# Kernel tuning notes

Measured on AMD Instinct MI355X. Metric: run time of the kernel, lower is better.

## Reference

```python
import jax, jax.numpy as jnp
import numpy as np

B = 16384
EPS = 1e-5
DIMS = [(3072, 4096), (4096, 4096), (4096, 256), (256, 16), (16, 16), (16, 10)]


def binarize(v):
    # BNN binarization with straight-through semantics (matches .data assignment in torch)
    return v + jax.lax.stop_gradient(jnp.sign(v) - v)


def blinear(x, w, b):
    # BinarizeLinear: binarize input (in_dim != 784) and weights, float bias add
    return binarize(x) @ binarize(w).T + b


def batchnorm(x, g, b):
    m = x.mean(axis=0)
    v = x.var(axis=0)
    return (x - m) * jax.lax.rsqrt(v + EPS) * g + b


def hardtanh(x):
    return jnp.clip(x, -1.0, 1.0)


def setup_inputs() -> dict:
    key = jax.random.key(0)
    ks = jax.random.split(key, 20)
    inp = {"x": jax.random.normal(ks[0], (B, 3072), dtype=jnp.float32)}
    for i, (din, dout) in enumerate(DIMS):
        inp[f"w{i}"] = jax.random.normal(ks[1 + 2 * i], (dout, din), dtype=jnp.float32) * 0.05
        inp[f"b{i}"] = jax.random.normal(ks[2 + 2 * i], (dout,), dtype=jnp.float32) * 0.01
    # BatchNorm affine params for layers after blinear 0,1,2 and final (dims 4096,4096,256,10)
    for j, d in enumerate([4096, 4096, 256, 10]):
        inp[f"g{j}"] = jnp.ones((d,), dtype=jnp.float32)
        inp[f"be{j}"] = jnp.zeros((d,), dtype=jnp.float32)
    return inp


def reference(x, w0, b0, w1, b1, w2, b2, w3, b3, w4, b4, w5, b5,
              g0, be0, g1, be1, g2, be2, g3, be3):
    h = x.reshape(-1, 3072)
    h = hardtanh(batchnorm(blinear(h, w0, b0), g0, be0))
    h = hardtanh(batchnorm(blinear(h, w1, b1), g1, be1))
    h = hardtanh(batchnorm(blinear(h, w2, b2), g2, be2))
    h = hardtanh(blinear(h, w3, b3))
    h = hardtanh(blinear(h, w4, b4))
    h = batchnorm(blinear(h, w5, b5), g3, be3)
    return jax.nn.log_softmax(h, axis=-1)
```

## Files before the change

### kernel.cpp

```cpp
#include <hip/hip_runtime.h>
#include <stdint.h>

typedef int v4i __attribute__((ext_vector_type(4)));
typedef int v8i __attribute__((ext_vector_type(8)));
typedef float v4f __attribute__((ext_vector_type(4)));
typedef short v8s __attribute__((ext_vector_type(8)));
typedef unsigned long long ull;
typedef unsigned int uint;

#define GLOAD16(g, l)                                                          \
  __builtin_amdgcn_global_load_lds(                                            \
      (const __attribute__((address_space(1))) void*)(g),                      \
      (__attribute__((address_space(3))) void*)(l), 16, 0, 0)

__device__ __forceinline__ signed char sgnf(float v) {
  return v > 0.f ? (signed char)1 : (v < 0.f ? (signed char)-1 : (signed char)0);
}
__device__ __forceinline__ uint nib(float v) {
  return v > 0.f ? 2u : (v < 0.f ? 10u : 0u);
}

__global__ void k_bin(const float4* __restrict__ in, char4* __restrict__ out, int n4) {
  int i = blockIdx.x * blockDim.x + threadIdx.x;
  int stride = gridDim.x * blockDim.x;
  for (; i < n4; i += stride) {
    float4 v = in[i];
    char4 o;
    o.x = sgnf(v.x); o.y = sgnf(v.y); o.z = sgnf(v.z); o.w = sgnf(v.w);
    out[i] = o;
  }
}

__global__ void k_binp(const float4* __restrict__ in, uint* __restrict__ out, int n8) {
  int i = blockIdx.x * blockDim.x + threadIdx.x;
  int stride = gridDim.x * blockDim.x;
  for (; i < n8; i += stride) {
    float4 a = in[i * 2], b = in[i * 2 + 1];
    out[i] = nib(a.x) | (nib(a.y) << 4) | (nib(a.z) << 8) | (nib(a.w) << 12) |
             (nib(b.x) << 16) | (nib(b.y) << 20) | (nib(b.z) << 24) | (nib(b.w) << 28);
  }
}

#define BM 128
#define BN 128

template <int K, int N>
__global__ __launch_bounds__(256, 2) void k_bgemm(
    const unsigned char* __restrict__ X, const unsigned char* __restrict__ W,
    short* __restrict__ A, ull* __restrict__ S, int M)
{
  __shared__ __align__(16) unsigned char As[BM * 128];
  __shared__ __align__(16) unsigned char Bs[BN * 128];
  constexpr int Kb = K >> 1;
  constexpr int NT = K / 256;
  constexpr int NBX = N / BN;
  const int t = threadIdx.x;
  const int lane = t & 63;
  const int wave = t >> 6;
  const int wm = wave >> 1, wn = wave & 1;

  const int wg = blockIdx.x;
  const int bm = (wg / NBX) * BM, bn = (wg % NBX) * BN;

  const int srow = lane >> 3;
  const int sslot = (lane & 7);

  const unsigned char* Xb0 = X + (size_t)bm * Kb;
  const unsigned char* Wb0 = W + (size_t)bn * Kb;

  v4f acc[4][4] = {};
  v8i a8[4], b8[4];
#pragma unroll
  for (int m = 0; m < 4; ++m) { a8[m] = (v8i)(0); b8[m] = (v8i)(0); }

  const unsigned char* gx[4];
  const unsigned char* gw[4];
  int ldsoff[4];
#pragma unroll
  for (int c = 0; c < 4; ++c) {
    int br = (wave * 4 + c) * 8;
    int row = br + srow;
    int ss = sslot ^ (row & 7);
    gx[c] = Xb0 + (size_t)row * Kb + ss * 16;
    gw[c] = Wb0 + (size_t)row * Kb + ss * 16;
    ldsoff[c] = br * 128;
  }
  int aoff[4], boff[4];
#pragma unroll
  for (int m = 0; m < 4; ++m) {
    int arow = wm * 64 + m * 16 + (lane & 15);
    aoff[m] = arow * 128 + (((lane >> 4) ^ (arow & 7)) * 16);
    int brow = wn * 64 + m * 16 + (lane & 15);
    boff[m] = brow * 128 + (((lane >> 4) ^ (brow & 7)) * 16);
  }

#pragma unroll
  for (int tile = 0; tile < NT; ++tile) {
#pragma unroll
    for (int c = 0; c < 4; ++c) {
      GLOAD16(gx[c] + tile * 128, As + ldsoff[c]);
      GLOAD16(gw[c] + tile * 128, Bs + ldsoff[c]);
    }
    __syncthreads();
#pragma unroll
    for (int kk = 0; kk < 2; ++kk) {
#pragma unroll
      for (int m = 0; m < 4; ++m) {
        v4i tmp = *(const v4i*)(As + (aoff[m] ^ (kk << 6)));
        a8[m][0] = tmp[0]; a8[m][1] = tmp[1]; a8[m][2] = tmp[2]; a8[m][3] = tmp[3];
      }
#pragma unroll
      for (int n = 0; n < 4; ++n) {
        v4i tmp = *(const v4i*)(Bs + (boff[n] ^ (kk << 6)));
        b8[n][0] = tmp[0]; b8[n][1] = tmp[1]; b8[n][2] = tmp[2]; b8[n][3] = tmp[3];
      }
#pragma unroll
      for (int m = 0; m < 4; ++m)
#pragma unroll
        for (int n = 0; n < 4; ++n)
          acc[m][n] = __builtin_amdgcn_mfma_scale_f32_16x16x128_f8f6f4(
              a8[m], b8[n], acc[m][n], 4 , 4 ,
              0, 0x7F7F7F7Fu, 0, 0x7F7F7F7Fu);
    }
    __syncthreads();
  }

#pragma unroll
  for (int m = 0; m < 4; ++m) {
    int rbase = bm + wm * 64 + m * 16 + (lane >> 4) * 4;
#pragma unroll
    for (int n = 0; n < 4; ++n) {
      int col = bn + wn * 64 + n * 16 + (lane & 15);
#pragma unroll
      for (int r = 0; r < 4; ++r)
        __builtin_nontemporal_store((short)(int)acc[m][n][r],
                                    A + (size_t)(rbase + r) * N + col);
    }
  }

#pragma unroll
  for (int n = 0; n < 4; ++n) {
    int s = 0, q = 0;
#pragma unroll
    for (int m = 0; m < 4; ++m)
#pragma unroll
      for (int r = 0; r < 4; ++r) {
        int v = (int)acc[m][n][r];
        s += v; q += v * v;
      }
    s += __shfl_xor(s, 16); s += __shfl_xor(s, 32);
    q += __shfl_xor(q, 16); q += __shfl_xor(q, 32);
    if ((lane >> 4) == 0) {
      int col = bn + wn * 64 + n * 16 + (lane & 15);
      atomicAdd(&S[col], (ull)(long long)s);
      atomicAdd(&S[(size_t)N + col], (ull)(long long)q);
    }
  }
}

__global__ void k_finalize(const ull* __restrict__ sums, const float* __restrict__ g,
                           int M, int N, float* __restrict__ meanf, float* __restrict__ sgf) {
  int j = blockIdx.x * blockDim.x + threadIdx.x;
  if (j >= N) return;
  double sum = (double)(long long)sums[j];
  double sumsq = (double)(long long)sums[N + j];
  double mean = sum / (double)M;
  double var = sumsq / (double)M - mean * mean;
  if (var < 0.0) var = 0.0;
  double inv = 1.0 / sqrt(var + 1e-5);
  meanf[j] = (float)mean;
  sgf[j] = (float)(inv * (double)g[j]);
}

__global__ void k_signbn_pack(const short* __restrict__ A, const float* __restrict__ meanf,
                              const float* __restrict__ sgf, const float* __restrict__ be,
                              uint* __restrict__ Xp, int total8, int nmask) {
  int i = blockIdx.x * blockDim.x + threadIdx.x;
  int stride = gridDim.x * blockDim.x;
  for (; i < total8; i += stride) {
    v8s a = __builtin_nontemporal_load((const v8s*)(A + (size_t)i * 8));
    int c0 = (i * 8) & nmask;
    uint b = 0;
#pragma unroll
    for (int j = 0; j < 8; ++j) {
      float z = ((float)a[j] - meanf[c0 + j]) * sgf[c0 + j] + be[c0 + j];
      b |= nib(z) << (4 * j);
    }
    Xp[i] = b;
  }
}

__global__ void k_signbn(const short4* __restrict__ A4, const float* __restrict__ meanf,
                         const float* __restrict__ sgf, const float* __restrict__ be,
                         char4* __restrict__ X4, int total4, int nmask) {
  int i = blockIdx.x * blockDim.x + threadIdx.x;
  int stride = gridDim.x * blockDim.x;
  for (; i < total4; i += stride) {
    short4 a = A4[i];
    int c0 = (i * 4) & nmask;
    char4 o;
    o.x = sgnf(((float)a.x - meanf[c0    ]) * sgf[c0    ] + be[c0    ]);
    o.y = sgnf(((float)a.y - meanf[c0 + 1]) * sgf[c0 + 1] + be[c0 + 1]);
    o.z = sgnf(((float)a.z - meanf[c0 + 2]) * sgf[c0 + 2] + be[c0 + 2]);
    o.w = sgnf(((float)a.w - meanf[c0 + 3]) * sgf[c0 + 3] + be[c0 + 3]);
    X4[i] = o;
  }
}

__global__ __launch_bounds__(256) void k_tail(
    const signed char* __restrict__ X3, const signed char* __restrict__ W3,
    const signed char* __restrict__ W4, const signed char* __restrict__ W5,
    const float* __restrict__ b3, const float* __restrict__ b4,
    int* __restrict__ A5, ull* __restrict__ sums5, int M)
{
  __shared__ __align__(16) signed char sW3[16 * 256];
  __shared__ __align__(16) signed char sW4[256];
  __shared__ __align__(16) signed char sW5[160];
  __shared__ __align__(16) signed char sX[16 * 256];
  __shared__ signed char sH[16][16];
  __shared__ int bsum[10], bsq[10];
  int t = threadIdx.x;
  int rowBlock = blockIdx.x * 16;
  ((int4*)sW3)[t] = ((const int4*)W3)[t];
  ((int4*)sX)[t] = ((const int4*)(X3 + (size_t)rowBlock * 256))[t];
  if (t < 16) ((int4*)sW4)[t] = ((const int4*)W4)[t];
  if (t < 10) {
    ((int4*)sW5)[t] = ((const int4*)W5)[t];
    bsum[t] = 0; bsq[t] = 0;
  }
  __syncthreads();
  int r = t >> 4, j = t & 15;
  int d3 = 0;
#pragma unroll 8
  for (int k = 0; k < 256; ++k) d3 += (int)sX[r * 256 + k] * (int)sW3[j * 256 + k];
  sH[r][j] = sgnf((float)d3 + b3[j]);
  __syncthreads();
  int d4 = 0;
#pragma unroll
  for (int k = 0; k < 16; ++k) d4 += (int)sH[r][k] * (int)sW4[j * 16 + k];
  signed char x5 = sgnf((float)d4 + b4[j]);
  __syncthreads();
  sH[r][j] = x5;
  __syncthreads();
  if (j < 10) {
    int d5 = 0;
#pragma unroll
    for (int k = 0; k < 16; ++k) d5 += (int)sH[r][k] * (int)sW5[j * 16 + k];
    A5[(size_t)(rowBlock + r) * 10 + j] = d5;
    atomicAdd(&bsum[j], d5);
    atomicAdd(&bsq[j], d5 * d5);
  }
  __syncthreads();
  if (t < 10) {
    atomicAdd(&sums5[t], (ull)(long long)bsum[t]);
    atomicAdd(&sums5[10 + t], (ull)(long long)bsq[t]);
  }
}

__global__ void k_lsm(const int* __restrict__ A5, const float* __restrict__ meanf,
                      const float* __restrict__ sgf, const float* __restrict__ be,
                      float* __restrict__ out, int M) {
  int r = blockIdx.x * blockDim.x + threadIdx.x;
  if (r >= M) return;
  float tv[10]; float mx = -3.0e38f;
#pragma unroll
  for (int j = 0; j < 10; ++j) {
    tv[j] = ((float)A5[(size_t)r * 10 + j] - meanf[j]) * sgf[j] + be[j];
    mx = fmaxf(mx, tv[j]);
  }
  float s = 0.f;
#pragma unroll
  for (int j = 0; j < 10; ++j) s += expf(tv[j] - mx);
  float lse = mx + logf(s);
#pragma unroll
  for (int j = 0; j < 10; ++j) out[(size_t)r * 10 + j] = tv[j] - lse;
}

extern "C" void kernel_launch(void* const* d_in, const int* in_sizes, int n_in,
                              void* d_out, int out_size, void* d_ws, size_t ws_size,
                              hipStream_t stream) {
  const float* x   = (const float*)d_in[0];
  const float* w0f = (const float*)d_in[1];
  const float* w1f = (const float*)d_in[3];
  const float* w2f = (const float*)d_in[5];
  const float* w3f = (const float*)d_in[7];  const float* b3f = (const float*)d_in[8];
  const float* w4f = (const float*)d_in[9];  const float* b4f = (const float*)d_in[10];
  const float* w5f = (const float*)d_in[11];
  const float* g0 = (const float*)d_in[13]; const float* be0 = (const float*)d_in[14];
  const float* g1 = (const float*)d_in[15]; const float* be1 = (const float*)d_in[16];
  const float* g2 = (const float*)d_in[17]; const float* be2 = (const float*)d_in[18];
  const float* g3 = (const float*)d_in[19]; const float* be3 = (const float*)d_in[20];

  const int M = in_sizes[0] / 3072;
  char* w = (char*)d_ws;
  short* Abuf          = (short*)w;
  unsigned char* X0p   = (unsigned char*)(w + 134217728);
  unsigned char* Xbp   = (unsigned char*)(w + 184549376);
  signed char* X3      = (signed char*)(w + 251658240);
  unsigned char* Ws0p  = (unsigned char*)(w + 255852544);
  unsigned char* Ws1p  = (unsigned char*)(w + 268435456);
  unsigned char* Ws2p  = (unsigned char*)(w + 285212672);
  signed char* Ws3 = (signed char*)(w + 286261248);
  signed char* Ws4 = (signed char*)(w + 286265344);
  signed char* Ws5 = (signed char*)(w + 286265600);
  int* A5          = (int*)(w + 286265856);
  ull* S0          = (ull*)(w + 286921216);
  ull* S1          = (ull*)(w + 286986752);
  ull* S2          = (ull*)(w + 287052288);
  ull* S5          = (ull*)(w + 287056384);
  float* P0m = (float*)(w + 287056640); float* P0s = (float*)(w + 287073024);
  float* P1m = (float*)(w + 287089408); float* P1s = (float*)(w + 287105792);
  float* P2m = (float*)(w + 287122176); float* P2s = (float*)(w + 287123200);
  float* P5m = (float*)(w + 287124224); float* P5s = (float*)(w + 287124288);

  hipMemsetAsync(w + 286921216, 0, 135424, stream);

  auto binp = [&](const float* src, unsigned char* dst, int n) {
    int n8 = n / 8;
    int grid = (n8 + 255) / 256; if (grid > 8192) grid = 8192;
    k_binp<<<grid, 256, 0, stream>>>((const float4*)src, (uint*)dst, n8);
  };
  binp(x,   X0p,  M * 3072);
  binp(w0f, Ws0p, 4096 * 3072);
  binp(w1f, Ws1p, 4096 * 4096);
  binp(w2f, Ws2p, 256 * 4096);
  k_bin<<<1, 64, 0, stream>>>((const float4*)w3f, (char4*)Ws3, 16 * 256 / 4);
  k_bin<<<1, 64, 0, stream>>>((const float4*)w4f, (char4*)Ws4, 16 * 16 / 4);
  k_bin<<<1, 40, 0, stream>>>((const float4*)w5f, (char4*)Ws5, 10 * 16 / 4);

  k_bgemm<3072, 4096><<<(4096 / BN) * (M / BM), 256, 0, stream>>>(X0p, Ws0p, Abuf, S0, M);
  k_finalize<<<16, 256, 0, stream>>>(S0, g0, M, 4096, P0m, P0s);
  k_signbn_pack<<<8192, 256, 0, stream>>>(Abuf, P0m, P0s, be0, (uint*)Xbp, M * 4096 / 8, 4095);

  k_bgemm<4096, 4096><<<(4096 / BN) * (M / BM), 256, 0, stream>>>(Xbp, Ws1p, Abuf, S1, M);
  k_finalize<<<16, 256, 0, stream>>>(S1, g1, M, 4096, P1m, P1s);
  k_signbn_pack<<<8192, 256, 0, stream>>>(Abuf, P1m, P1s, be1, (uint*)Xbp, M * 4096 / 8, 4095);

  k_bgemm<4096, 256><<<(256 / BN) * (M / BM), 256, 0, stream>>>(Xbp, Ws2p, Abuf, S2, M);
  k_finalize<<<1, 256, 0, stream>>>(S2, g2, M, 256, P2m, P2s);
  k_signbn<<<4096, 256, 0, stream>>>((const short4*)Abuf, P2m, P2s, be2, (char4*)X3, M * 256 / 4, 255);

  k_tail<<<M / 16, 256, 0, stream>>>(X3, Ws3, Ws4, Ws5, b3f, b4f, A5, S5, M);
  k_finalize<<<1, 32, 0, stream>>>(S5, g3, M, 10, P5m, P5s);
  k_lsm<<<(M + 255) / 256, 256, 0, stream>>>(A5, P5m, P5s, be3, (float*)d_out, M);

  (void)n_in; (void)out_size; (void)ws_size;
}
```

Measured before the change: 481.7 us.

## Add 256x256 8-wave FP4 GEMM with double-buffered LDS pipeline for big layers

```diff
diff --git a/kernel.cpp b/kernel.cpp
--- a/kernel.cpp
+++ b/kernel.cpp
@@ -12,6 +12,12 @@
   __builtin_amdgcn_global_load_lds(                                            \
       (const __attribute__((address_space(1))) void*)(g),                      \
       (__attribute__((address_space(3))) void*)(l), 16, 0, 0)
+
+__device__ __forceinline__ void bar() {
+  asm volatile("" ::: "memory");
+  __builtin_amdgcn_s_barrier();
+  asm volatile("" ::: "memory");
+}
 
 __device__ __forceinline__ signed char sgnf(float v) {
   return v > 0.f ? (signed char)1 : (v < 0.f ? (signed char)-1 : (signed char)0);
@@ -38,6 +44,161 @@
     float4 a = in[i * 2], b = in[i * 2 + 1];
     out[i] = nib(a.x) | (nib(a.y) << 4) | (nib(a.z) << 8) | (nib(a.w) << 12) |
              (nib(b.x) << 16) | (nib(b.y) << 20) | (nib(b.z) << 24) | (nib(b.w) << 28);
+  }
+}
+
+#define BM2 256
+#define BN2 256
+
+template <int K, int N>
+__global__ __launch_bounds__(512, 2) void k_bgemm2(
+    const unsigned char* __restrict__ X, const unsigned char* __restrict__ W,
+    short* __restrict__ A, ull* __restrict__ S, int M)
+{
+  __shared__ __align__(16) unsigned char lds[2][2][BM2 * 128];
+  constexpr int Kb = K >> 1;
+  constexpr int NT = K / 256;
+  constexpr int NBX = N / BN2;
+  const int t512 = threadIdx.x;
+  const int lane = t512 & 63;
+  const int wave = t512 >> 6;
+  const int wm = wave >> 2;
+  const int wn = wave & 3;
+  const int wg = blockIdx.x;
+  const int bm = (wg / NBX) * BM2, bn = (wg % NBX) * BN2;
+
+  const int srow = lane >> 3;
+  const int ssl = (lane & 7) ^ (srow & 7);
+
+  const unsigned char* gA[2][2];
+  const unsigned char* gB[2][2];
+  int ldst[2][2];
+#pragma unroll
+  for (int h = 0; h < 2; ++h)
+#pragma unroll
+    for (int c = 0; c < 2; ++c) {
+      int row = h * 128 + c * 64 + wave * 8 + srow;
+      gA[h][c] = X + (size_t)(bm + row) * Kb + ssl * 16;
+      gB[h][c] = W + (size_t)(bn + row) * Kb + ssl * 16;
+      ldst[h][c] = (h * 128 + c * 64 + wave * 8) * 128;
+    }
+
+  auto stageA = [&](int h, int buf, int tt) {
+    GLOAD16(gA[h][0] + tt * 128, &lds[buf][0][ldst[h][0]]);
+    GLOAD16(gA[h][1] + tt * 128, &lds[buf][0][ldst[h][1]]);
+  };
+  auto stageB = [&](int h, int buf, int tt) {
+    GLOAD16(gB[h][0] + tt * 128, &lds[buf][1][ldst[h][0]]);
+    GLOAD16(gB[h][1] + tt * 128, &lds[buf][1][ldst[h][1]]);
+  };
+
+  int aoff[8], boff[4];
+#pragma unroll
+  for (int m = 0; m < 8; ++m) {
+    int r = wm * 128 + m * 16 + (lane & 15);
+    aoff[m] = r * 128 + (((lane >> 4) ^ (r & 7)) * 16);
+  }
+#pragma unroll
+  for (int n = 0; n < 4; ++n) {
+    int r = wn * 64 + n * 16 + (lane & 15);
+    boff[n] = r * 128 + (((lane >> 4) ^ (r & 7)) * 16);
+  }
+
+  v4f acc[8][4] = {};
+  v8i a8[4][2], b8[4][2];
+#pragma unroll
+  for (int i = 0; i < 4; ++i)
+#pragma unroll
+    for (int kk = 0; kk < 2; ++kk) { a8[i][kk] = (v8i)(0); b8[i][kk] = (v8i)(0); }
+
+#define RD_A(mh, Ap)                                                           \
+  _Pragma("unroll") for (int mq = 0; mq < 4; ++mq)                             \
+    _Pragma("unroll") for (int kk = 0; kk < 2; ++kk) {                         \
+      v4i tmp = *(const v4i*)((Ap) + (aoff[(mh) * 4 + mq] ^ (kk << 6)));       \
+      a8[mq][kk][0] = tmp[0]; a8[mq][kk][1] = tmp[1];                          \
+      a8[mq][kk][2] = tmp[2]; a8[mq][kk][3] = tmp[3]; }
+#define RD_B(nh, Bp)                                                           \
+  _Pragma("unroll") for (int nq = 0; nq < 2; ++nq)                             \
+    _Pragma("unroll") for (int kk = 0; kk < 2; ++kk) {                         \
+      v4i tmp = *(const v4i*)((Bp) + (boff[(nh) * 2 + nq] ^ (kk << 6)));       \
+      b8[(nh) * 2 + nq][kk][0] = tmp[0]; b8[(nh) * 2 + nq][kk][1] = tmp[1];    \
+      b8[(nh) * 2 + nq][kk][2] = tmp[2]; b8[(nh) * 2 + nq][kk][3] = tmp[3]; }
+#define QUAD(mh, nh)                                                           \
+  { __builtin_amdgcn_s_setprio(1);                                             \
+    _Pragma("unroll") for (int mq = 0; mq < 4; ++mq)                           \
+      _Pragma("unroll") for (int nq = 0; nq < 2; ++nq)                         \
+        _Pragma("unroll") for (int kk = 0; kk < 2; ++kk)                       \
+          acc[(mh) * 4 + mq][(nh) * 2 + nq] =                                  \
+              __builtin_amdgcn_mfma_scale_f32_16x16x128_f8f6f4(                \
+                  a8[mq][kk], b8[(nh) * 2 + nq][kk],                           \
+                  acc[(mh) * 4 + mq][(nh) * 2 + nq],                           \
+                  4, 4, 0, 0x7F7F7F7Fu, 0, 0x7F7F7F7Fu);                       \
+    __builtin_amdgcn_s_setprio(0); }
+
+  stageA(0, 0, 0); stageB(0, 0, 0); stageA(1, 0, 0); stageB(1, 0, 0);
+  stageB(0, 1, 1); stageA(0, 1, 1);
+  asm volatile("s_waitcnt vmcnt(4)" ::: "memory");
+  bar();
+
+#pragma unroll 2
+  for (int t = 0; t < NT; ++t) {
+    const int p = t & 1, q = p ^ 1;
+    const unsigned char* Ap = &lds[p][0][0];
+    const unsigned char* Bp = &lds[p][1][0];
+    RD_A(0, Ap); RD_B(0, Bp);
+    if (t + 1 < NT) stageA(1, q, t + 1);
+    bar(); QUAD(0, 0); bar();
+    RD_B(1, Bp);
+    if (t + 1 < NT) stageB(1, q, t + 1);
+    bar(); QUAD(0, 1); bar();
+    RD_A(1, Ap);
+    if (t + 2 < NT) stageB(0, p, t + 2);
+    bar(); QUAD(1, 0); bar();
+    if (t + 2 < NT) {
+      stageA(0, p, t + 2);
+      asm volatile("s_waitcnt vmcnt(4)" ::: "memory");
+    } else {
+      asm volatile("s_waitcnt vmcnt(0)" ::: "memory");
+    }
+    bar(); QUAD(1, 1); bar();
+  }
+#undef RD_A
+#undef RD_B
+#undef QUAD
+
+#pragma unroll
+  for (int m = 0; m < 8; ++m) {
+    int rbase = bm + wm * 128 + m * 16 + (lane >> 4) * 4;
+#pragma unroll
+    for (int n = 0; n < 4; ++n) {
+      int col = bn + wn * 64 + n * 16 + (lane & 15);
+#pragma unroll
+      for (int r = 0; r < 4; ++r)
+        __builtin_nontemporal_store((short)(int)acc[m][n][r],
+                                    A + (size_t)(rbase + r) * N + col);
+    }
+  }
+
+#pragma unroll
+  for (int n = 0; n < 4; ++n) {
+    int s = 0; long long q64 = 0;
+#pragma unroll
+    for (int m = 0; m < 8; ++m) {
+      int qq = 0;
+#pragma unroll
+      for (int r = 0; r < 4; ++r) {
+        int v = (int)acc[m][n][r];
+        s += v; qq += v * v;
+      }
+      q64 += qq;
+    }
+    s += __shfl_xor(s, 16); s += __shfl_xor(s, 32);
+    q64 += __shfl_xor(q64, 16); q64 += __shfl_xor(q64, 32);
+    if ((lane >> 4) == 0) {
+      int col = bn + wn * 64 + n * 16 + (lane & 15);
+      atomicAdd(&S[col], (ull)(long long)s);
+      atomicAdd(&S[(size_t)N + col], (ull)q64);
+    }
   }
 }
 
@@ -58,7 +219,6 @@
   const int lane = t & 63;
   const int wave = t >> 6;
   const int wm = wave >> 1, wn = wave & 1;
-
   const int wg = blockIdx.x;
   const int bm = (wg / NBX) * BM, bn = (wg % NBX) * BN;
 
@@ -119,8 +279,7 @@
 #pragma unroll
         for (int n = 0; n < 4; ++n)
           acc[m][n] = __builtin_amdgcn_mfma_scale_f32_16x16x128_f8f6f4(
-              a8[m], b8[n], acc[m][n], 4 , 4 ,
-              0, 0x7F7F7F7Fu, 0, 0x7F7F7F7Fu);
+              a8[m], b8[n], acc[m][n], 4, 4, 0, 0x7F7F7F7Fu, 0, 0x7F7F7F7Fu);
     }
     __syncthreads();
   }
@@ -328,11 +487,11 @@
   k_bin<<<1, 64, 0, stream>>>((const float4*)w4f, (char4*)Ws4, 16 * 16 / 4);
   k_bin<<<1, 40, 0, stream>>>((const float4*)w5f, (char4*)Ws5, 10 * 16 / 4);
 
-  k_bgemm<3072, 4096><<<(4096 / BN) * (M / BM), 256, 0, stream>>>(X0p, Ws0p, Abuf, S0, M);
+  k_bgemm2<3072, 4096><<<(4096 / BN2) * (M / BM2), 512, 0, stream>>>(X0p, Ws0p, Abuf, S0, M);
   k_finalize<<<16, 256, 0, stream>>>(S0, g0, M, 4096, P0m, P0s);
   k_signbn_pack<<<8192, 256, 0, stream>>>(Abuf, P0m, P0s, be0, (uint*)Xbp, M * 4096 / 8, 4095);
 
-  k_bgemm<4096, 4096><<<(4096 / BN) * (M / BM), 256, 0, stream>>>(Xbp, Ws1p, Abuf, S1, M);
+  k_bgemm2<4096, 4096><<<(4096 / BN2) * (M / BM2), 512, 0, stream>>>(Xbp, Ws1p, Abuf, S1, M);
   k_finalize<<<16, 256, 0, stream>>>(S1, g1, M, 4096, P1m, P1s);
   k_signbn_pack<<<8192, 256, 0, stream>>>(Abuf, P1m, P1s, be1, (uint*)Xbp, M * 4096 / 8, 4095);
 
```

New measurement: 1.701 ms. +253.1%, slower.
